# Performance work log

Hardware: AMD Instinct MI355X
Metric: run time of the kernel (lower is better)

## Reference

```python
import jax, jax.numpy as jnp
import numpy as np

N_NODES = 100000
N_EDGES = 1600000
N_GRAPHS = 2048
IN_DIM = 128
HIDDEN = 128
OUT_DIM = 3


def setup_inputs() -> dict:
    key = jax.random.key(0)
    ks = jax.random.split(key, 16)
    x = jax.random.normal(ks[0], (N_NODES, IN_DIM), dtype=jnp.float32)
    edge_index = jax.random.randint(ks[1], (2, N_EDGES), 0, N_NODES, dtype=jnp.int64)
    batch = jnp.sort(jax.random.randint(ks[2], (N_NODES,), 0, N_GRAPHS, dtype=jnp.int64))
    s = 0.02
    return {
        "x": x,
        "edge_index": edge_index,
        "batch": batch,
        # GINConv MLP: Linear(in,hidden) -> ReLU -> Linear(hidden,hidden)
        "gin_w1": jax.random.normal(ks[3], (IN_DIM, HIDDEN), dtype=jnp.float32) * s,
        "gin_b1": jnp.zeros((HIDDEN,), dtype=jnp.float32),
        "gin_w2": jax.random.normal(ks[4], (HIDDEN, HIDDEN), dtype=jnp.float32) * s,
        "gin_b2": jnp.zeros((HIDDEN,), dtype=jnp.float32),
        # GCNConv weight + bias
        "gcn_w": jax.random.normal(ks[5], (HIDDEN, HIDDEN), dtype=jnp.float32) * s,
        "gcn_b": jnp.zeros((HIDDEN,), dtype=jnp.float32),
        # head
        "lin1_w": jax.random.normal(ks[6], (HIDDEN, HIDDEN), dtype=jnp.float32) * s,
        "lin1_b": jnp.zeros((HIDDEN,), dtype=jnp.float32),
        "lin2_w": jax.random.normal(ks[7], (HIDDEN, OUT_DIM), dtype=jnp.float32) * s,
        "lin2_b": jnp.zeros((OUT_DIM,), dtype=jnp.float32),
    }


def reference(x, edge_index, batch, gin_w1, gin_b1, gin_w2, gin_b2,
              gcn_w, gcn_b, lin1_w, lin1_b, lin2_w, lin2_b):
    src, dst = edge_index[0], edge_index[1]

    # ---- GINConv (eps=0): h_i = MLP(x_i + sum_{j in N(i)} x_j) ----
    agg = jax.ops.segment_sum(x[src], dst, num_segments=N_NODES)  # [N, in_dim]
    h = agg + x  # (1 + eps) * x with eps = 0
    h = jax.nn.relu(h @ gin_w1 + gin_b1) @ gin_w2 + gin_b2
    h = jax.nn.relu(h)  # outer F.relu

    # ---- GCNConv with self-loops and symmetric normalization ----
    # deg_i = (# incoming edges to i) + 1 (self-loop)
    ones_e = jnp.ones((N_EDGES,), dtype=h.dtype)
    deg = jax.ops.segment_sum(ones_e, dst, num_segments=N_NODES) + 1.0
    dinv = jax.lax.rsqrt(deg)  # deg >= 1 always
    hw = h @ gcn_w  # [N, hidden]
    norm_e = dinv[src] * dinv[dst]  # [E]
    msg = jax.ops.segment_sum(norm_e[:, None] * hw[src], dst, num_segments=N_NODES)
    h = msg + (dinv * dinv)[:, None] * hw + gcn_b  # self-loop contribution
    h = jax.nn.relu(h)

    # ---- global_add_pool over graphs ----
    g = jax.ops.segment_sum(h, batch, num_segments=N_GRAPHS)  # [G, hidden]

    g = jax.nn.relu(g @ lin1_w + lin1_b)
    return g @ lin2_w + lin2_b  # [G, out_dim]
```

## Files before the change

### kernel.cpp

```cpp
#include <hip/hip_runtime.h>
#include <hip/hip_bf16.h>

#define N_NODES  100000
#define N_EDGES  1600000
#define N_GRAPHS 2048
#define DIM      128
#define ELLW     64

__device__ __forceinline__ unsigned short f2b(float f) {
    unsigned u = __float_as_uint(f);
    u += 0x7FFFu + ((u >> 16) & 1u);
    return (unsigned short)(u >> 16);
}
__device__ __forceinline__ float b2f(unsigned short h) {
    return __uint_as_float(((unsigned)h) << 16);
}
__device__ __forceinline__ float4 dec4(ushort4 h) {
    return make_float4(b2f(h.x), b2f(h.y), b2f(h.z), b2f(h.w));
}

typedef __attribute__((ext_vector_type(8))) short bfrag;
typedef __attribute__((ext_vector_type(4))) float ffrag;

__global__ __launch_bounds__(256)
void cast_bf16(const float* __restrict__ in, unsigned short* __restrict__ out,
               int* __restrict__ cursor,
               const float* __restrict__ Wa, unsigned short* __restrict__ Ta,
               const float* __restrict__ Wb, unsigned short* __restrict__ Tb,
               const float* __restrict__ Wc, unsigned short* __restrict__ Tc,
               int n8)
{
    int i = blockIdx.x * 256 + threadIdx.x;
    if (i < N_NODES) cursor[i] = 0;
    if (i < 3 * DIM * DIM) {
        int which = i >> 14;
        int idx   = i & (DIM * DIM - 1);
        const float* W = (which == 0) ? Wa : (which == 1) ? Wb : Wc;
        unsigned short* T = (which == 0) ? Ta : (which == 1) ? Tb : Tc;
        int k = idx >> 7, n = idx & 127;
        T[n * DIM + k] = f2b(W[idx]);
    }
    if (i >= n8) return;
    const float4* in4 = (const float4*)in;
    float4 a = in4[i * 2 + 0];
    float4 b = in4[i * 2 + 1];
    uint4 q;
    q.x = (unsigned)f2b(a.x) | ((unsigned)f2b(a.y) << 16);
    q.y = (unsigned)f2b(a.z) | ((unsigned)f2b(a.w) << 16);
    q.z = (unsigned)f2b(b.x) | ((unsigned)f2b(b.y) << 16);
    q.w = (unsigned)f2b(b.z) | ((unsigned)f2b(b.w) << 16);
    ((uint4*)out)[i] = q;
}

#define FILL_RANGES 8
#define FILL_RSIZE  (N_NODES / FILL_RANGES)

__global__ __launch_bounds__(256)
void ell_fill(const int* __restrict__ src, const int* __restrict__ dst,
              int* __restrict__ cursor, int* __restrict__ ell,
              float* __restrict__ g, int E)
{
    int gid = blockIdx.x * 256 + threadIdx.x;
    g[gid] = 0.f;

    const int r = blockIdx.x & (FILL_RANGES - 1);
    const int s = blockIdx.x >> 3;
    const int nslice = gridDim.x >> 3;
    const unsigned lo = (unsigned)(r * FILL_RSIZE);
    const int stride = nslice * 256 * 4;

    for (int e0 = (s * 256 + threadIdx.x) * 4; e0 < E; e0 += stride) {
        int4 d  = *(const int4*)&dst[e0];
        int4 sv = *(const int4*)&src[e0];
        if ((unsigned)(d.x - lo) < (unsigned)FILL_RSIZE) {
            int p = atomicAdd(&cursor[d.x], 1); ell[d.x * ELLW + p] = sv.x;
        }
        if ((unsigned)(d.y - lo) < (unsigned)FILL_RSIZE) {
            int p = atomicAdd(&cursor[d.y], 1); ell[d.y * ELLW + p] = sv.y;
        }
        if ((unsigned)(d.z - lo) < (unsigned)FILL_RSIZE) {
            int p = atomicAdd(&cursor[d.z], 1); ell[d.z * ELLW + p] = sv.z;
        }
        if ((unsigned)(d.w - lo) < (unsigned)FILL_RSIZE) {
            int p = atomicAdd(&cursor[d.w], 1); ell[d.w * ELLW + p] = sv.w;
        }
    }
}

__global__ __launch_bounds__(256)
void ell_gather_bb(const int* __restrict__ deg, const int* __restrict__ ell,
                   const unsigned short* __restrict__ Vb,
                   unsigned short* __restrict__ Out,
                   float* __restrict__ dinv, int N)
{
    int node = blockIdx.x * 8 + (threadIdx.x >> 5);
    int lane = threadIdx.x & 31;
    if (node >= N) return;
    int dn = deg[node];
    if (lane == 0) dinv[node] = rsqrtf((float)dn + 1.0f);
    const int* row = ell + node * ELLW;
    const ushort4* V4 = (const ushort4*)Vb;
    float4 acc = dec4(V4[(size_t)node * 32 + lane]);
    int e = 0;
    for (; e + 8 <= dn; e += 8) {
        int s0 = row[e + 0], s1 = row[e + 1], s2 = row[e + 2], s3 = row[e + 3];
        int s4 = row[e + 4], s5 = row[e + 5], s6 = row[e + 6], s7 = row[e + 7];
        float4 v0 = dec4(V4[(size_t)s0 * 32 + lane]);
        float4 v1 = dec4(V4[(size_t)s1 * 32 + lane]);
        float4 v2 = dec4(V4[(size_t)s2 * 32 + lane]);
        float4 v3 = dec4(V4[(size_t)s3 * 32 + lane]);
        float4 v4 = dec4(V4[(size_t)s4 * 32 + lane]);
        float4 v5 = dec4(V4[(size_t)s5 * 32 + lane]);
        float4 v6 = dec4(V4[(size_t)s6 * 32 + lane]);
        float4 v7 = dec4(V4[(size_t)s7 * 32 + lane]);
        acc.x += (v0.x + v1.x + v2.x + v3.x) + (v4.x + v5.x + v6.x + v7.x);
        acc.y += (v0.y + v1.y + v2.y + v3.y) + (v4.y + v5.y + v6.y + v7.y);
        acc.z += (v0.z + v1.z + v2.z + v3.z) + (v4.z + v5.z + v6.z + v7.z);
        acc.w += (v0.w + v1.w + v2.w + v3.w) + (v4.w + v5.w + v6.w + v7.w);
    }
    for (; e + 4 <= dn; e += 4) {
        int s0 = row[e + 0], s1 = row[e + 1], s2 = row[e + 2], s3 = row[e + 3];
        float4 v0 = dec4(V4[(size_t)s0 * 32 + lane]);
        float4 v1 = dec4(V4[(size_t)s1 * 32 + lane]);
        float4 v2 = dec4(V4[(size_t)s2 * 32 + lane]);
        float4 v3 = dec4(V4[(size_t)s3 * 32 + lane]);
        acc.x += v0.x + v1.x + v2.x + v3.x;
        acc.y += v0.y + v1.y + v2.y + v3.y;
        acc.z += v0.z + v1.z + v2.z + v3.z;
        acc.w += v0.w + v1.w + v2.w + v3.w;
    }
    for (; e < dn; ++e) {
        int s = row[e];
        float4 v = dec4(V4[(size_t)s * 32 + lane]);
        acc.x += v.x; acc.y += v.y; acc.z += v.z; acc.w += v.w;
    }
    ushort4 o;
    o.x = f2b(acc.x); o.y = f2b(acc.y); o.z = f2b(acc.z); o.w = f2b(acc.w);
    ((ushort4*)Out)[(size_t)node * 32 + lane] = o;
}

#define MLP_ROWS 64
#define HBST     136

__global__ __launch_bounds__(256)
void mlp3_mfma(const unsigned short* __restrict__ Hg,
               const unsigned short* __restrict__ w1t, const float* __restrict__ b1,
               const unsigned short* __restrict__ w2t, const float* __restrict__ b2,
               const unsigned short* __restrict__ w3t, const float* __restrict__ dinv,
               unsigned short* __restrict__ ub_out, int N)
{
    __shared__ unsigned short Hb[MLP_ROWS][HBST];
    __shared__ unsigned short Ws[DIM][HBST];

    const int tid  = threadIdx.x;
    const int wave = tid >> 6;
    const int lane = tid & 63;
    const int row0 = blockIdx.x * MLP_ROWS;

#pragma unroll
    for (int l = 0; l < 4; ++l) {
        int f  = tid + l * 256;
        int r  = f >> 4;
        int c8 = (f & 15) << 3;
        int gr = row0 + r;
        uint4 v = make_uint4(0u, 0u, 0u, 0u);
        if (gr < N) v = *(const uint4*)&Hg[(size_t)gr * DIM + c8];
        *(uint4*)&Hb[r][c8] = v;
    }

    const int m0 = wave * 16;
    const int qa = lane >> 4;
    const int la = lane & 15;

    for (int layer = 0; layer < 3; ++layer) {
        const unsigned short* __restrict__ Wt =
            (layer == 0) ? w1t : (layer == 1) ? w2t : w3t;

        __syncthreads();
#pragma unroll
        for (int l = 0; l < 8; ++l) {
            int f  = tid + l * 256;
            int r  = f >> 4;
            int c8 = (f & 15) << 3;
            *(uint4*)&Ws[r][c8] = *(const uint4*)&Wt[(size_t)r * DIM + c8];
        }
        __syncthreads();

        bfrag afr[4];
#pragma unroll
        for (int kc = 0; kc < 4; ++kc)
            afr[kc] = *(const bfrag*)&Hb[m0 + la][kc * 32 + qa * 8];

        if (layer < 2) {
            const float* bias = (layer == 0) ? b1 : b2;
#pragma unroll
            for (int nt = 0; nt < 8; ++nt) {
                const int n0 = nt * 16;
                ffrag acc = {0.f, 0.f, 0.f, 0.f};
#pragma unroll
                for (int kc = 0; kc < 4; ++kc) {
                    bfrag bfr = *(const bfrag*)&Ws[n0 + la][kc * 32 + qa * 8];
                    acc = __builtin_amdgcn_mfma_f32_16x16x32_bf16(afr[kc], bfr, acc, 0, 0, 0);
                }
                float bn = bias[n0 + la];
#pragma unroll
                for (int r = 0; r < 4; ++r) {
                    float v = fmaxf(acc[r] + bn, 0.f);
                    Hb[m0 + qa * 4 + r][n0 + la] = f2b(v);
                }
            }
        } else {
            float dv[4];
#pragma unroll
            for (int r = 0; r < 4; ++r) {
                int gr = row0 + m0 + qa * 4 + r;
                dv[r] = (gr < N) ? dinv[gr] : 0.f;
            }
#pragma unroll
            for (int nt = 0; nt < 8; ++nt) {
                const int n0 = nt * 16;
                ffrag acc = {0.f, 0.f, 0.f, 0.f};
#pragma unroll
                for (int kc = 0; kc < 4; ++kc) {
                    bfrag bfr = *(const bfrag*)&Ws[n0 + la][kc * 32 + qa * 8];
                    acc = __builtin_amdgcn_mfma_f32_16x16x32_bf16(afr[kc], bfr, acc, 0, 0, 0);
                }
#pragma unroll
                for (int r = 0; r < 4; ++r) {
                    int gr = row0 + m0 + qa * 4 + r;
                    if (gr < N)
                        ub_out[(size_t)gr * DIM + n0 + la] = f2b(dv[r] * acc[r]);
                }
            }
        }
    }
}

#define P2_NODES 64
__global__ __launch_bounds__(256)
void gcn_gather_pool(const int* __restrict__ deg, const int* __restrict__ ell,
                     const unsigned short* __restrict__ ub,
                     const float* __restrict__ dinv,
                     const float* __restrict__ bias, const int* __restrict__ batch,
                     float* __restrict__ g, int N)
{
    const int grp  = threadIdx.x >> 5;
    const int lane = threadIdx.x & 31;
    const int n0   = blockIdx.x * P2_NODES + grp * 8;
    const ushort4* V4 = (const ushort4*)ub;

    float4 bj;
    bj.x = bias[lane * 4 + 0];
    bj.y = bias[lane * 4 + 1];
    bj.z = bias[lane * 4 + 2];
    bj.w = bias[lane * 4 + 3];

    float4 lsum = make_float4(0.f, 0.f, 0.f, 0.f);
    int prev = -1;

    for (int k = 0; k < 8; ++k) {
        int node = n0 + k;
        if (node >= N) break;
        int dn = deg[node];
        const int* row = ell + node * ELLW;
        float4 acc = dec4(V4[(size_t)node * 32 + lane]);
        int e = 0;
        for (; e + 8 <= dn; e += 8) {
            int s0 = row[e + 0], s1 = row[e + 1], s2 = row[e + 2], s3 = row[e + 3];
            int s4 = row[e + 4], s5 = row[e + 5], s6 = row[e + 6], s7 = row[e + 7];
            float4 v0 = dec4(V4[(size_t)s0 * 32 + lane]);
            float4 v1 = dec4(V4[(size_t)s1 * 32 + lane]);
            float4 v2 = dec4(V4[(size_t)s2 * 32 + lane]);
            float4 v3 = dec4(V4[(size_t)s3 * 32 + lane]);
            float4 v4 = dec4(V4[(size_t)s4 * 32 + lane]);
            float4 v5 = dec4(V4[(size_t)s5 * 32 + lane]);
            float4 v6 = dec4(V4[(size_t)s6 * 32 + lane]);
            float4 v7 = dec4(V4[(size_t)s7 * 32 + lane]);
            acc.x += (v0.x + v1.x + v2.x + v3.x) + (v4.x + v5.x + v6.x + v7.x);
            acc.y += (v0.y + v1.y + v2.y + v3.y) + (v4.y + v5.y + v6.y + v7.y);
            acc.z += (v0.z + v1.z + v2.z + v3.z) + (v4.z + v5.z + v6.z + v7.z);
            acc.w += (v0.w + v1.w + v2.w + v3.w) + (v4.w + v5.w + v6.w + v7.w);
        }
        for (; e + 4 <= dn; e += 4) {
            int s0 = row[e + 0], s1 = row[e + 1], s2 = row[e + 2], s3 = row[e + 3];
            float4 v0 = dec4(V4[(size_t)s0 * 32 + lane]);
            float4 v1 = dec4(V4[(size_t)s1 * 32 + lane]);
            float4 v2 = dec4(V4[(size_t)s2 * 32 + lane]);
            float4 v3 = dec4(V4[(size_t)s3 * 32 + lane]);
            acc.x += v0.x + v1.x + v2.x + v3.x;
            acc.y += v0.y + v1.y + v2.y + v3.y;
            acc.z += v0.z + v1.z + v2.z + v3.z;
            acc.w += v0.w + v1.w + v2.w + v3.w;
        }
        for (; e < dn; ++e) {
            int s = row[e];
            float4 v = dec4(V4[(size_t)s * 32 + lane]);
            acc.x += v.x; acc.y += v.y; acc.z += v.z; acc.w += v.w;
        }
        float di = dinv[node];
        float4 h;
        h.x = fmaxf(fmaf(di, acc.x, bj.x), 0.f);
        h.y = fmaxf(fmaf(di, acc.y, bj.y), 0.f);
        h.z = fmaxf(fmaf(di, acc.z, bj.z), 0.f);
        h.w = fmaxf(fmaf(di, acc.w, bj.w), 0.f);

        int b = batch[node];
        if (b != prev) {
            if (prev >= 0) {
                float* gp = &g[(size_t)prev * DIM + lane * 4];
                atomicAdd(gp + 0, lsum.x);
                atomicAdd(gp + 1, lsum.y);
                atomicAdd(gp + 2, lsum.z);
                atomicAdd(gp + 3, lsum.w);
            }
            lsum = make_float4(0.f, 0.f, 0.f, 0.f);
            prev = b;
        }
        lsum.x += h.x; lsum.y += h.y; lsum.z += h.z; lsum.w += h.w;
    }
    if (prev >= 0) {
        float* gp = &g[(size_t)prev * DIM + lane * 4];
        atomicAdd(gp + 0, lsum.x);
        atomicAdd(gp + 1, lsum.y);
        atomicAdd(gp + 2, lsum.z);
        atomicAdd(gp + 3, lsum.w);
    }
}

__global__ __launch_bounds__(128)
void head_kernel(const float* __restrict__ g, const float* __restrict__ w1,
                 const float* __restrict__ b1, const float* __restrict__ w2,
                 const float* __restrict__ b2, float* __restrict__ out)
{
    __shared__ float gs[DIM];
    __shared__ float red[6];
    int gid = blockIdx.x;
    int t = threadIdx.x;

    gs[t] = g[(size_t)gid * DIM + t];
    __syncthreads();

    float acc = b1[t];
#pragma unroll
    for (int k = 0; k < DIM; ++k) acc = fmaf(gs[k], w1[k * DIM + t], acc);
    float h = fmaxf(acc, 0.f);

    float c0 = h * w2[t * 3 + 0];
    float c1 = h * w2[t * 3 + 1];
    float c2 = h * w2[t * 3 + 2];
#pragma unroll
    for (int off = 32; off >= 1; off >>= 1) {
        c0 += __shfl_down(c0, off);
        c1 += __shfl_down(c1, off);
        c2 += __shfl_down(c2, off);
    }
    int wave = t >> 6;
    if ((t & 63) == 0) {
        red[wave * 3 + 0] = c0;
        red[wave * 3 + 1] = c1;
        red[wave * 3 + 2] = c2;
    }
    __syncthreads();
    if (t == 0) {
        out[(size_t)gid * 3 + 0] = red[0] + red[3] + b2[0];
        out[(size_t)gid * 3 + 1] = red[1] + red[4] + b2[1];
        out[(size_t)gid * 3 + 2] = red[2] + red[5] + b2[2];
    }
}

extern "C" void kernel_launch(void* const* d_in, const int* in_sizes, int n_in,
                              void* d_out, int out_size, void* d_ws, size_t ws_size,
                              hipStream_t stream)
{
    const float* x       = (const float*)d_in[0];
    const int*   eidx    = (const int*)d_in[1];
    const int*   batch   = (const int*)d_in[2];
    const float* gin_w1  = (const float*)d_in[3];
    const float* gin_b1  = (const float*)d_in[4];
    const float* gin_w2  = (const float*)d_in[5];
    const float* gin_b2  = (const float*)d_in[6];
    const float* gcn_w   = (const float*)d_in[7];
    const float* gcn_b   = (const float*)d_in[8];
    const float* lin1_w  = (const float*)d_in[9];
    const float* lin1_b  = (const float*)d_in[10];
    const float* lin2_w  = (const float*)d_in[11];
    const float* lin2_b  = (const float*)d_in[12];

    const int* src = eidx;
    const int* dst = eidx + N_EDGES;

    const size_t NBH = (size_t)N_NODES * DIM * sizeof(unsigned short);
    const size_t WTB = (size_t)DIM * DIM * sizeof(unsigned short);
    char* base = (char*)d_ws;
    size_t off = 0;
    auto carve = [&](size_t bytes) {
        char* p = base + off;
        off = (off + bytes + 255) & ~(size_t)255;
        return p;
    };
    unsigned short* xb  = (unsigned short*)carve(NBH);
    unsigned short* hb  = (unsigned short*)carve(NBH);
    unsigned short* ub  = (unsigned short*)carve(NBH);
    unsigned short* w1t = (unsigned short*)carve(WTB);
    unsigned short* w2t = (unsigned short*)carve(WTB);
    unsigned short* w3t = (unsigned short*)carve(WTB);
    int*   cursor = (int*)  carve(N_NODES * sizeof(int));
    int*   ell    = (int*)  carve((size_t)N_NODES * ELLW * sizeof(int));
    float* dinv   = (float*)carve(N_NODES * sizeof(float));
    float* g      = (float*)carve((size_t)N_GRAPHS * DIM * sizeof(float));

    const int ngrid = (N_NODES + 7) / 8;
    const int mgrid = (N_NODES + MLP_ROWS - 1) / MLP_ROWS;
    const int pgrid = (N_NODES + P2_NODES - 1) / P2_NODES;

    cast_bf16<<<(N_NODES * DIM / 8 + 255) / 256, 256, 0, stream>>>(
        x, xb, cursor, gin_w1, w1t, gin_w2, w2t, gcn_w, w3t,
        N_NODES * DIM / 8);

    ell_fill<<<FILL_RANGES * 128, 256, 0, stream>>>(src, dst, cursor, ell,
                                                    g, N_EDGES);

    ell_gather_bb<<<ngrid, 256, 0, stream>>>(cursor, ell, xb, hb, dinv, N_NODES);

    mlp3_mfma<<<mgrid, 256, 0, stream>>>(hb, w1t, gin_b1, w2t, gin_b2,
                                         w3t, dinv, ub, N_NODES);

    gcn_gather_pool<<<pgrid, 256, 0, stream>>>(cursor, ell, ub, dinv, gcn_b,
                                               batch, g, N_NODES);

    head_kernel<<<N_GRAPHS, 128, 0, stream>>>(
        g, lin1_w, lin1_b, lin2_w, lin2_b, (float*)d_out);
}
```

Baseline: 367.5 us.

## Fuse GIN neighbor gather into MLP kernel and recompute dinv on the fly

The ELL neighbor-sum for GINConv now runs inside the MFMA MLP kernel. Each 32-lane group aggregates 8 rows straight into shared memory, so the bf16 intermediate buffer no longer has to be written to and read back from global memory, and one kernel launch goes away. The dinv array is dropped: it is kept in shared memory for the MLP's last layer and recomputed from the degree in the GCN gather kernel. In exchange, the latency-bound gather now runs inside a kernel whose large shared-memory footprint limits occupancy. That can reduce how well memory latency is hidden during the irregular loads.

```diff
diff --git a/kernel.cpp b/kernel.cpp
--- a/kernel.cpp
+++ b/kernel.cpp
@@ -87,87 +87,77 @@
     }
 }
 
-__global__ __launch_bounds__(256)
-void ell_gather_bb(const int* __restrict__ deg, const int* __restrict__ ell,
-                   const unsigned short* __restrict__ Vb,
-                   unsigned short* __restrict__ Out,
-                   float* __restrict__ dinv, int N)
-{
-    int node = blockIdx.x * 8 + (threadIdx.x >> 5);
-    int lane = threadIdx.x & 31;
-    if (node >= N) return;
-    int dn = deg[node];
-    if (lane == 0) dinv[node] = rsqrtf((float)dn + 1.0f);
-    const int* row = ell + node * ELLW;
-    const ushort4* V4 = (const ushort4*)Vb;
-    float4 acc = dec4(V4[(size_t)node * 32 + lane]);
-    int e = 0;
-    for (; e + 8 <= dn; e += 8) {
-        int s0 = row[e + 0], s1 = row[e + 1], s2 = row[e + 2], s3 = row[e + 3];
-        int s4 = row[e + 4], s5 = row[e + 5], s6 = row[e + 6], s7 = row[e + 7];
-        float4 v0 = dec4(V4[(size_t)s0 * 32 + lane]);
-        float4 v1 = dec4(V4[(size_t)s1 * 32 + lane]);
-        float4 v2 = dec4(V4[(size_t)s2 * 32 + lane]);
-        float4 v3 = dec4(V4[(size_t)s3 * 32 + lane]);
-        float4 v4 = dec4(V4[(size_t)s4 * 32 + lane]);
-        float4 v5 = dec4(V4[(size_t)s5 * 32 + lane]);
-        float4 v6 = dec4(V4[(size_t)s6 * 32 + lane]);
-        float4 v7 = dec4(V4[(size_t)s7 * 32 + lane]);
-        acc.x += (v0.x + v1.x + v2.x + v3.x) + (v4.x + v5.x + v6.x + v7.x);
-        acc.y += (v0.y + v1.y + v2.y + v3.y) + (v4.y + v5.y + v6.y + v7.y);
-        acc.z += (v0.z + v1.z + v2.z + v3.z) + (v4.z + v5.z + v6.z + v7.z);
-        acc.w += (v0.w + v1.w + v2.w + v3.w) + (v4.w + v5.w + v6.w + v7.w);
-    }
-    for (; e + 4 <= dn; e += 4) {
-        int s0 = row[e + 0], s1 = row[e + 1], s2 = row[e + 2], s3 = row[e + 3];
-        float4 v0 = dec4(V4[(size_t)s0 * 32 + lane]);
-        float4 v1 = dec4(V4[(size_t)s1 * 32 + lane]);
-        float4 v2 = dec4(V4[(size_t)s2 * 32 + lane]);
-        float4 v3 = dec4(V4[(size_t)s3 * 32 + lane]);
-        acc.x += v0.x + v1.x + v2.x + v3.x;
-        acc.y += v0.y + v1.y + v2.y + v3.y;
-        acc.z += v0.z + v1.z + v2.z + v3.z;
-        acc.w += v0.w + v1.w + v2.w + v3.w;
-    }
-    for (; e < dn; ++e) {
-        int s = row[e];
-        float4 v = dec4(V4[(size_t)s * 32 + lane]);
-        acc.x += v.x; acc.y += v.y; acc.z += v.z; acc.w += v.w;
-    }
-    ushort4 o;
-    o.x = f2b(acc.x); o.y = f2b(acc.y); o.z = f2b(acc.z); o.w = f2b(acc.w);
-    ((ushort4*)Out)[(size_t)node * 32 + lane] = o;
-}
-
 #define MLP_ROWS 64
 #define HBST     136
 
 __global__ __launch_bounds__(256)
-void mlp3_mfma(const unsigned short* __restrict__ Hg,
-               const unsigned short* __restrict__ w1t, const float* __restrict__ b1,
-               const unsigned short* __restrict__ w2t, const float* __restrict__ b2,
-               const unsigned short* __restrict__ w3t, const float* __restrict__ dinv,
-               unsigned short* __restrict__ ub_out, int N)
+void mlp3_fused(const int* __restrict__ deg, const int* __restrict__ ell,
+                const unsigned short* __restrict__ xb,
+                const unsigned short* __restrict__ w1t, const float* __restrict__ b1,
+                const unsigned short* __restrict__ w2t, const float* __restrict__ b2,
+                const unsigned short* __restrict__ w3t,
+                unsigned short* __restrict__ ub_out, int N)
 {
     __shared__ unsigned short Hb[MLP_ROWS][HBST];
     __shared__ unsigned short Ws[DIM][HBST];
+    __shared__ float dvs[MLP_ROWS];
 
     const int tid  = threadIdx.x;
+    const int row0 = blockIdx.x * MLP_ROWS;
+
+    {
+        const int grp = tid >> 5;
+        const int gl  = tid & 31;
+        const ushort4* V4 = (const ushort4*)xb;
+        for (int k = 0; k < 8; ++k) {
+            int r = grp * 8 + k;
+            int node = row0 + r;
+            if (node >= N) break;
+            int dn = deg[node];
+            if (gl == 0) dvs[r] = rsqrtf((float)dn + 1.0f);
+            const int* row = ell + (size_t)node * ELLW;
+            float4 acc = dec4(V4[(size_t)node * 32 + gl]);
+            int e = 0;
+            for (; e + 8 <= dn; e += 8) {
+                int s0 = row[e + 0], s1 = row[e + 1], s2 = row[e + 2], s3 = row[e + 3];
+                int s4 = row[e + 4], s5 = row[e + 5], s6 = row[e + 6], s7 = row[e + 7];
+                float4 v0 = dec4(V4[(size_t)s0 * 32 + gl]);
+                float4 v1 = dec4(V4[(size_t)s1 * 32 + gl]);
+                float4 v2 = dec4(V4[(size_t)s2 * 32 + gl]);
+                float4 v3 = dec4(V4[(size_t)s3 * 32 + gl]);
+                float4 v4 = dec4(V4[(size_t)s4 * 32 + gl]);
+                float4 v5 = dec4(V4[(size_t)s5 * 32 + gl]);
+                float4 v6 = dec4(V4[(size_t)s6 * 32 + gl]);
+                float4 v7 = dec4(V4[(size_t)s7 * 32 + gl]);
+                acc.x += (v0.x + v1.x + v2.x + v3.x) + (v4.x + v5.x + v6.x + v7.x);
+                acc.y += (v0.y + v1.y + v2.y + v3.y) + (v4.y + v5.y + v6.y + v7.y);
+                acc.z += (v0.z + v1.z + v2.z + v3.z) + (v4.z + v5.z + v6.z + v7.z);
+                acc.w += (v0.w + v1.w + v2.w + v3.w) + (v4.w + v5.w + v6.w + v7.w);
+            }
+            for (; e + 4 <= dn; e += 4) {
+                int s0 = row[e + 0], s1 = row[e + 1], s2 = row[e + 2], s3 = row[e + 3];
+                float4 v0 = dec4(V4[(size_t)s0 * 32 + gl]);
+                float4 v1 = dec4(V4[(size_t)s1 * 32 + gl]);
+                float4 v2 = dec4(V4[(size_t)s2 * 32 + gl]);
+                float4 v3 = dec4(V4[(size_t)s3 * 32 + gl]);
+                acc.x += v0.x + v1.x + v2.x + v3.x;
+                acc.y += v0.y + v1.y + v2.y + v3.y;
+                acc.z += v0.z + v1.z + v2.z + v3.z;
+                acc.w += v0.w + v1.w + v2.w + v3.w;
+            }
+            for (; e < dn; ++e) {
+                int s = row[e];
+                float4 v = dec4(V4[(size_t)s * 32 + gl]);
+                acc.x += v.x; acc.y += v.y; acc.z += v.z; acc.w += v.w;
+            }
+            ushort4 o;
+            o.x = f2b(acc.x); o.y = f2b(acc.y); o.z = f2b(acc.z); o.w = f2b(acc.w);
+            *(ushort4*)&Hb[r][gl * 4] = o;
+        }
+    }
+
     const int wave = tid >> 6;
     const int lane = tid & 63;
-    const int row0 = blockIdx.x * MLP_ROWS;
-
-#pragma unroll
-    for (int l = 0; l < 4; ++l) {
-        int f  = tid + l * 256;
-        int r  = f >> 4;
-        int c8 = (f & 15) << 3;
-        int gr = row0 + r;
-        uint4 v = make_uint4(0u, 0u, 0u, 0u);
-        if (gr < N) v = *(const uint4*)&Hg[(size_t)gr * DIM + c8];
-        *(uint4*)&Hb[r][c8] = v;
-    }
-
     const int m0 = wave * 16;
     const int qa = lane >> 4;
     const int la = lane & 15;
@@ -212,10 +202,8 @@
         } else {
             float dv[4];
 #pragma unroll
-            for (int r = 0; r < 4; ++r) {
-                int gr = row0 + m0 + qa * 4 + r;
-                dv[r] = (gr < N) ? dinv[gr] : 0.f;
-            }
+            for (int r = 0; r < 4; ++r)
+                dv[r] = dvs[m0 + qa * 4 + r];
 #pragma unroll
             for (int nt = 0; nt < 8; ++nt) {
                 const int n0 = nt * 16;
@@ -240,7 +228,6 @@
 __global__ __launch_bounds__(256)
 void gcn_gather_pool(const int* __restrict__ deg, const int* __restrict__ ell,
                      const unsigned short* __restrict__ ub,
-                     const float* __restrict__ dinv,
                      const float* __restrict__ bias, const int* __restrict__ batch,
                      float* __restrict__ g, int N)
 {
@@ -297,7 +284,7 @@
             float4 v = dec4(V4[(size_t)s * 32 + lane]);
             acc.x += v.x; acc.y += v.y; acc.z += v.z; acc.w += v.w;
         }
-        float di = dinv[node];
+        float di = rsqrtf((float)dn + 1.0f);
         float4 h;
         h.x = fmaxf(fmaf(di, acc.x, bj.x), 0.f);
         h.y = fmaxf(fmaf(di, acc.y, bj.y), 0.f);
@@ -399,17 +386,14 @@
         return p;
     };
     unsigned short* xb  = (unsigned short*)carve(NBH);
-    unsigned short* hb  = (unsigned short*)carve(NBH);
     unsigned short* ub  = (unsigned short*)carve(NBH);
     unsigned short* w1t = (unsigned short*)carve(WTB);
     unsigned short* w2t = (unsigned short*)carve(WTB);
     unsigned short* w3t = (unsigned short*)carve(WTB);
     int*   cursor = (int*)  carve(N_NODES * sizeof(int));
     int*   ell    = (int*)  carve((size_t)N_NODES * ELLW * sizeof(int));
-    float* dinv   = (float*)carve(N_NODES * sizeof(float));
     float* g      = (float*)carve((size_t)N_GRAPHS * DIM * sizeof(float));
 
-    const int ngrid = (N_NODES + 7) / 8;
     const int mgrid = (N_NODES + MLP_ROWS - 1) / MLP_ROWS;
     const int pgrid = (N_NODES + P2_NODES - 1) / P2_NODES;
 
@@ -420,12 +404,10 @@
     ell_fill<<<FILL_RANGES * 128, 256, 0, stream>>>(src, dst, cursor, ell,
                                                     g, N_EDGES);
 
-    ell_gather_bb<<<ngrid, 256, 0, stream>>>(cursor, ell, xb, hb, dinv, N_NODES);
-
-    mlp3_mfma<<<mgrid, 256, 0, stream>>>(hb, w1t, gin_b1, w2t, gin_b2,
-                                         w3t, dinv, ub, N_NODES);
-
-    gcn_gather_pool<<<pgrid, 256, 0, stream>>>(cursor, ell, ub, dinv, gcn_b,
+    mlp3_fused<<<mgrid, 256, 0, stream>>>(cursor, ell, xb, w1t, gin_b1,
+                                          w2t, gin_b2, w3t, ub, N_NODES);
+
+    gcn_gather_pool<<<pgrid, 256, 0, stream>>>(cursor, ell, ub, gcn_b,
                                                batch, g, N_NODES);
 
     head_kernel<<<N_GRAPHS, 128, 0, stream>>>(
```

Result: slower. 395.6 us (+7.7%).
